# Kernel optimization log

Hardware: AMD Instinct MI355X
Metric: run time of the kernel (lower is better)

The kernel has to match this reference:

```python
import jax, jax.numpy as jnp
import numpy as np

N_NODES = 100000
N_EDGES = 3200000
D_IN, D_HID, D_OUT = 64, 16, 32


def setup_inputs() -> dict:
    key = jax.random.key(0)
    k1, k2, k3, k4, k5 = jax.random.split(key, 5)
    x = jax.random.normal(k1, (N_NODES, D_IN), dtype=jnp.float32)
    edge_index = jax.random.randint(k2, (2, N_EDGES), 0, N_NODES, dtype=jnp.int64)
    edge_weight = jax.random.uniform(k3, (N_EDGES,), dtype=jnp.float32)
    # Learned params (GCNConv lin has no bias; conv bias added post-aggregation)
    W_gcn = jax.random.normal(k4, (D_IN, D_HID), dtype=jnp.float32) / np.sqrt(D_IN)
    b_gcn = jnp.zeros((D_HID,), dtype=jnp.float32)
    W_out = jax.random.normal(k5, (D_HID, D_OUT), dtype=jnp.float32) / np.sqrt(D_HID)
    b_out = jnp.zeros((D_OUT,), dtype=jnp.float32)
    return {"x": x, "edge_index": edge_index, "edge_weight": edge_weight,
            "W_gcn": W_gcn, "b_gcn": b_gcn, "W_out": W_out, "b_out": b_out}


def reference(x, edge_index, edge_weight, W_gcn, b_gcn, W_out, b_out):
    N = x.shape[0]
    # --- gcn_norm with self loops (PyG defaults: add_self_loops=True, fill=1) ---
    loop = jnp.arange(N, dtype=edge_index.dtype)
    row = jnp.concatenate([edge_index[0], loop])  # source
    col = jnp.concatenate([edge_index[1], loop])  # target
    w = jnp.concatenate([edge_weight, jnp.ones((N,), dtype=x.dtype)])
    deg = jax.ops.segment_sum(w, col, num_segments=N)  # in-degree at targets
    dinv = jnp.where(deg > 0, jax.lax.rsqrt(deg), 0.0).astype(x.dtype)
    norm = dinv[row] * w * dinv[col]  # [E+N]
    # --- transform then gather / scatter-add aggregation ---
    h = x @ W_gcn                      # [N, 16]
    msg = h[row] * norm[:, None]       # [E+N, 16]
    agg = jax.ops.segment_sum(msg, col, num_segments=N) + b_gcn
    emb = jax.nn.relu(agg)
    return emb @ W_out + b_out         # [N, 32]
```

## Files before the change

### kernel.cpp

```cpp
#include <hip/hip_runtime.h>

#define D_IN  64
#define D_HID 16
#define D_OUT 32

#define CPB    64
#define CPB_SH 6
#define NB_MAX 1600
#define BINB   128

__global__ __launch_bounds__(256) void k_bincount(
        const int* __restrict__ col, int* __restrict__ cntB, int E, int NB) {
    __shared__ int hist[NB_MAX];
    for (int b = threadIdx.x; b < NB; b += 256) hist[b] = 0;
    __syncthreads();
    int chunk = (E + BINB - 1) / BINB;
    int s = blockIdx.x * chunk;
    int e = min(E, s + chunk);
    for (int i = s + threadIdx.x; i < e; i += 256)
        atomicAdd(&hist[col[i] >> CPB_SH], 1);
    __syncthreads();
    for (int b = threadIdx.x; b < NB; b += 256)
        cntB[b * BINB + blockIdx.x] = hist[b];
}

__global__ __launch_bounds__(BINB) void k_scanblk(int* __restrict__ cntB,
                                                  int* __restrict__ bb, int NB) {
    __shared__ int s[BINB];
    int b = blockIdx.x;
    int v = cntB[(size_t)b * BINB + threadIdx.x];
    s[threadIdx.x] = v;
    __syncthreads();
    for (int off = 1; off < BINB; off <<= 1) {
        int t = (threadIdx.x >= off) ? s[threadIdx.x - off] : 0;
        __syncthreads();
        s[threadIdx.x] += t;
        __syncthreads();
    }
    cntB[(size_t)b * BINB + threadIdx.x] = s[threadIdx.x] - v;
    if (threadIdx.x == BINB - 1) bb[b] = s[BINB - 1];
}

__global__ void k_scanbase(int* __restrict__ bb, int NB) {
    __shared__ int s[512];
    __shared__ int basev;
    if (threadIdx.x == 0) basev = 0;
    __syncthreads();
    for (int start = 0; start < NB; start += 512) {
        int idx = start + threadIdx.x;
        int v = (idx < NB) ? bb[idx] : 0;
        s[threadIdx.x] = v;
        __syncthreads();
        for (int off = 1; off < 512; off <<= 1) {
            int t = (threadIdx.x >= off) ? s[threadIdx.x - off] : 0;
            __syncthreads();
            s[threadIdx.x] += t;
            __syncthreads();
        }
        if (idx < NB) bb[idx] = basev + s[threadIdx.x] - v;
        __syncthreads();
        if (threadIdx.x == 0) basev += s[511];
        __syncthreads();
    }
    if (threadIdx.x == 0) bb[NB] = basev;
}

__global__ __launch_bounds__(256) void k_binfill(
        const int* __restrict__ ei, const float* __restrict__ w,
        const int* __restrict__ bb, const int* __restrict__ cntB,
        int2* __restrict__ binned, int E, int NB) {
    __shared__ int cur[NB_MAX];
    for (int b = threadIdx.x; b < NB; b += 256)
        cur[b] = bb[b] + cntB[(size_t)b * BINB + blockIdx.x];
    __syncthreads();
    int chunk = (E + BINB - 1) / BINB;
    int s = blockIdx.x * chunk;
    int e = min(E, s + chunk);
    for (int i = s + threadIdx.x; i < e; i += 256) {
        int c = ei[(size_t)E + i];
        int r = ei[i];
        float wt = w[i];
        int pos = atomicAdd(&cur[c >> CPB_SH], 1);
        binned[pos] = make_int2(r | ((c & (CPB - 1)) << 20), __float_as_int(wt));
    }
}

__global__ __launch_bounds__(256) void k_deg(
        const int2* __restrict__ binned, const int* __restrict__ bb,
        float* __restrict__ dinv, int N) {
    __shared__ float wsum[CPB];
    if (threadIdx.x < CPB) wsum[threadIdx.x] = 0.f;
    __syncthreads();
    int b = blockIdx.x;
    int s = bb[b], e = bb[b + 1];
    for (int i = s + threadIdx.x; i < e; i += 256) {
        int2 v = binned[i];
        atomicAdd(&wsum[(v.x >> 20) & (CPB - 1)], __int_as_float(v.y));
    }
    __syncthreads();
    if (threadIdx.x < CPB) {
        int n = (b << CPB_SH) + threadIdx.x;
        if (n < N) dinv[n] = rsqrtf(1.0f + wsum[threadIdx.x]);
    }
}

__global__ __launch_bounds__(256) void k_transform(
        const float4* __restrict__ x4,
        const float* __restrict__ Wg,
        const float* __restrict__ dinv,
        float* __restrict__ hs, int N) {
    __shared__ float Wl[D_IN * D_HID];
    __shared__ float xlf[16][68];
    for (int i = threadIdx.x; i < D_IN * D_HID; i += 256) Wl[i] = Wg[i];
    const int f = threadIdx.x & 15, nl = threadIdx.x >> 4;
    for (int base = blockIdx.x * 16; base < N; base += gridDim.x * 16) {
        __syncthreads();
        int n = base + nl;
        if (n < N) {
            float4 v = x4[(size_t)n * 16 + f];
            xlf[nl][f * 4 + 0] = v.x;
            xlf[nl][f * 4 + 1] = v.y;
            xlf[nl][f * 4 + 2] = v.z;
            xlf[nl][f * 4 + 3] = v.w;
        }
        __syncthreads();
        if (n < N) {
            float acc = 0.f;
#pragma unroll
            for (int k = 0; k < D_IN; ++k) acc += xlf[nl][k] * Wl[k * D_HID + f];
            hs[(size_t)n * D_HID + f] = acc * dinv[n];
        }
    }
}

__global__ __launch_bounds__(256) void k_aggout(
        const int2* __restrict__ binned, const int* __restrict__ bb,
        const float* __restrict__ hs, const float* __restrict__ dinv,
        const float* __restrict__ bg, const float* __restrict__ Wo,
        const float* __restrict__ bo, float* __restrict__ out, int N) {
    __shared__ float acc[CPB][D_HID + 1];
    __shared__ float Wl[D_HID * D_OUT];
    __shared__ float bgl[D_HID];
    __shared__ float bol[D_OUT];
    for (int i = threadIdx.x; i < CPB * (D_HID + 1); i += 256)
        ((float*)acc)[i] = 0.f;
    for (int i = threadIdx.x; i < D_HID * D_OUT; i += 256) Wl[i] = Wo[i];
    if (threadIdx.x < D_HID) bgl[threadIdx.x] = bg[threadIdx.x];
    if (threadIdx.x < D_OUT) bol[threadIdx.x] = bo[threadIdx.x];
    __syncthreads();

    int b = blockIdx.x;
    int s = bb[b], e = bb[b + 1];
    const int f = threadIdx.x & 15;
    int i = s + (threadIdx.x >> 4);
    for (; i + 16 < e; i += 32) {
        int2 v0 = binned[i];
        int2 v1 = binned[i + 16];
        float h0 = hs[(size_t)(v0.x & 0xFFFFF) * D_HID + f];
        float h1 = hs[(size_t)(v1.x & 0xFFFFF) * D_HID + f];
        atomicAdd(&acc[(v0.x >> 20) & (CPB - 1)][f], h0 * __int_as_float(v0.y));
        atomicAdd(&acc[(v1.x >> 20) & (CPB - 1)][f], h1 * __int_as_float(v1.y));
    }
    if (i < e) {
        int2 v = binned[i];
        float h = hs[(size_t)(v.x & 0xFFFFF) * D_HID + f];
        atomicAdd(&acc[(v.x >> 20) & (CPB - 1)][f], h * __int_as_float(v.y));
    }
    __syncthreads();

    {
        const int nl = threadIdx.x >> 4;
#pragma unroll
        for (int rep = 0; rep < CPB / 16; ++rep) {
            int cl = nl + rep * 16;
            int n = (b << CPB_SH) + cl;
            if (n < N) {
                float di = dinv[n];
                float v = di * (acc[cl][f] + hs[(size_t)n * D_HID + f]) + bgl[f];
                acc[cl][f] = fmaxf(v, 0.f);
            }
        }
    }
    __syncthreads();

    {
        const int o  = threadIdx.x & 31;
        const int n2 = threadIdx.x >> 5;
#pragma unroll
        for (int rep = 0; rep < CPB / 8; ++rep) {
            int cl = n2 + rep * 8;
            int n = (b << CPB_SH) + cl;
            if (n < N) {
                float a = bol[o];
#pragma unroll
                for (int ff = 0; ff < D_HID; ++ff)
                    a += acc[cl][ff] * Wl[ff * D_OUT + o];
                out[(size_t)n * D_OUT + o] = a;
            }
        }
    }
}

extern "C" void kernel_launch(void* const* d_in, const int* in_sizes, int n_in,
                              void* d_out, int out_size, void* d_ws, size_t ws_size,
                              hipStream_t stream) {
    const float* x  = (const float*)d_in[0];
    const int*   ei = (const int*)d_in[1];
    const float* ew = (const float*)d_in[2];
    const float* Wg = (const float*)d_in[3];
    const float* bg = (const float*)d_in[4];
    const float* Wo = (const float*)d_in[5];
    const float* bo = (const float*)d_in[6];
    float* out = (float*)d_out;

    const int N  = in_sizes[0] / D_IN;
    const int E  = in_sizes[2];
    const int NB = (N + CPB - 1) >> CPB_SH;

    float* ws    = (float*)d_ws;
    float* dinv  = ws;
    int*   bb    = (int*)(ws + N);
    size_t bbe   = (size_t)N + (size_t)((NB + 2) & ~1);
    int2*  binned = (int2*)(ws + bbe);
    float* hs    = ws + bbe + (size_t)2 * E;
    int*   cntB  = (int*)hs;

    k_bincount<<<BINB, 256, 0, stream>>>(ei + E, cntB, E, NB);
    k_scanblk <<<NB, BINB, 0, stream>>>(cntB, bb, NB);
    k_scanbase<<<1, 512, 0, stream>>>(bb, NB);
    k_binfill <<<BINB, 256, 0, stream>>>(ei, ew, bb, cntB, binned, E, NB);
    k_deg     <<<NB, 256, 0, stream>>>(binned, bb, dinv, N);
    k_transform<<<(N + 15) / 16, 256, 0, stream>>>((const float4*)x, Wg, dinv, hs, N);
    k_aggout  <<<NB, 256, 0, stream>>>(binned, bb, hs, dinv, bg, Wo, bo, out, N);
}
```

Before: 558.8 us.

## Bin edges by source band then target block, with nontemporal loads

Edges are now binned first by a band of the source node index (32768 nodes per band) and then by target block. Each aggregation block walks its bins band by band, so the gathered rows of hs from all blocks fall in a narrower address range at any given time, which is meant to improve cache locality. Streaming reads of edge_index, weights and binned entries now use nontemporal loads, and the binning grid is cut from 128 to 64 blocks. The trade-offs are a larger histogram (up to 6400 bins in LDS), more scan work, and fewer blocks in the bincount and binfill kernels.

New measurement: 728.8 us. +30.4%, slower.

```diff
diff --git a/kernel.cpp b/kernel.cpp
--- a/kernel.cpp
+++ b/kernel.cpp
@@ -4,28 +4,40 @@
 #define D_HID 16
 #define D_OUT 32
 
-#define CPB    64
-#define CPB_SH 6
-#define NB_MAX 1600
-#define BINB   128
+#define CPB      64
+#define CPB_SH   6
+#define BAND_SH  15
+#define NBIN_MAX 6400
+#define BINB     64
+
+static __device__ __forceinline__ long long ntld_ll(const void* p) {
+    return __builtin_nontemporal_load((const long long*)p);
+}
+static __device__ __forceinline__ int ntld_i(const int* p) {
+    return __builtin_nontemporal_load(p);
+}
 
 __global__ __launch_bounds__(256) void k_bincount(
-        const int* __restrict__ col, int* __restrict__ cntB, int E, int NB) {
-    __shared__ int hist[NB_MAX];
-    for (int b = threadIdx.x; b < NB; b += 256) hist[b] = 0;
+        const int* __restrict__ ei, int* __restrict__ cntB,
+        int E, int NB, int NBIN) {
+    __shared__ int hist[NBIN_MAX];
+    for (int b = threadIdx.x; b < NBIN; b += 256) hist[b] = 0;
     __syncthreads();
     int chunk = (E + BINB - 1) / BINB;
     int s = blockIdx.x * chunk;
     int e = min(E, s + chunk);
-    for (int i = s + threadIdx.x; i < e; i += 256)
-        atomicAdd(&hist[col[i] >> CPB_SH], 1);
-    __syncthreads();
-    for (int b = threadIdx.x; b < NB; b += 256)
-        cntB[b * BINB + blockIdx.x] = hist[b];
+    for (int i = s + threadIdx.x; i < e; i += 256) {
+        int r = ntld_i(ei + i);
+        int c = ntld_i(ei + E + i);
+        atomicAdd(&hist[(r >> BAND_SH) * NB + (c >> CPB_SH)], 1);
+    }
+    __syncthreads();
+    for (int b = threadIdx.x; b < NBIN; b += 256)
+        cntB[(size_t)b * BINB + blockIdx.x] = hist[b];
 }
 
 __global__ __launch_bounds__(BINB) void k_scanblk(int* __restrict__ cntB,
-                                                  int* __restrict__ bb, int NB) {
+                                                  int* __restrict__ bb, int NBIN) {
     __shared__ int s[BINB];
     int b = blockIdx.x;
     int v = cntB[(size_t)b * BINB + threadIdx.x];
@@ -41,14 +53,14 @@
     if (threadIdx.x == BINB - 1) bb[b] = s[BINB - 1];
 }
 
-__global__ void k_scanbase(int* __restrict__ bb, int NB) {
+__global__ void k_scanbase(int* __restrict__ bb, int NBIN) {
     __shared__ int s[512];
     __shared__ int basev;
     if (threadIdx.x == 0) basev = 0;
     __syncthreads();
-    for (int start = 0; start < NB; start += 512) {
+    for (int start = 0; start < NBIN; start += 512) {
         int idx = start + threadIdx.x;
-        int v = (idx < NB) ? bb[idx] : 0;
+        int v = (idx < NBIN) ? bb[idx] : 0;
         s[threadIdx.x] = v;
         __syncthreads();
         for (int off = 1; off < 512; off <<= 1) {
@@ -57,45 +69,49 @@
             s[threadIdx.x] += t;
             __syncthreads();
         }
-        if (idx < NB) bb[idx] = basev + s[threadIdx.x] - v;
+        if (idx < NBIN) bb[idx] = basev + s[threadIdx.x] - v;
         __syncthreads();
         if (threadIdx.x == 0) basev += s[511];
         __syncthreads();
     }
-    if (threadIdx.x == 0) bb[NB] = basev;
+    if (threadIdx.x == 0) bb[NBIN] = basev;
 }
 
 __global__ __launch_bounds__(256) void k_binfill(
         const int* __restrict__ ei, const float* __restrict__ w,
         const int* __restrict__ bb, const int* __restrict__ cntB,
-        int2* __restrict__ binned, int E, int NB) {
-    __shared__ int cur[NB_MAX];
-    for (int b = threadIdx.x; b < NB; b += 256)
+        int2* __restrict__ binned, int E, int NB, int NBIN) {
+    __shared__ int cur[NBIN_MAX];
+    for (int b = threadIdx.x; b < NBIN; b += 256)
         cur[b] = bb[b] + cntB[(size_t)b * BINB + blockIdx.x];
     __syncthreads();
     int chunk = (E + BINB - 1) / BINB;
     int s = blockIdx.x * chunk;
     int e = min(E, s + chunk);
     for (int i = s + threadIdx.x; i < e; i += 256) {
-        int c = ei[(size_t)E + i];
-        int r = ei[i];
-        float wt = w[i];
-        int pos = atomicAdd(&cur[c >> CPB_SH], 1);
+        int r = ntld_i(ei + i);
+        int c = ntld_i(ei + E + i);
+        float wt = __builtin_nontemporal_load(w + i);
+        int bin = (r >> BAND_SH) * NB + (c >> CPB_SH);
+        int pos = atomicAdd(&cur[bin], 1);
         binned[pos] = make_int2(r | ((c & (CPB - 1)) << 20), __float_as_int(wt));
     }
 }
 
 __global__ __launch_bounds__(256) void k_deg(
         const int2* __restrict__ binned, const int* __restrict__ bb,
-        float* __restrict__ dinv, int N) {
+        float* __restrict__ dinv, int N, int NB, int nband) {
     __shared__ float wsum[CPB];
     if (threadIdx.x < CPB) wsum[threadIdx.x] = 0.f;
     __syncthreads();
     int b = blockIdx.x;
-    int s = bb[b], e = bb[b + 1];
-    for (int i = s + threadIdx.x; i < e; i += 256) {
-        int2 v = binned[i];
-        atomicAdd(&wsum[(v.x >> 20) & (CPB - 1)], __int_as_float(v.y));
+    for (int band = 0; band < nband; ++band) {
+        int bs = bb[band * NB + b], be = bb[band * NB + b + 1];
+        for (int i = bs + threadIdx.x; i < be; i += 256) {
+            long long p = ntld_ll(binned + i);
+            atomicAdd(&wsum[((int)p >> 20) & (CPB - 1)],
+                      __int_as_float((int)(p >> 32)));
+        }
     }
     __syncthreads();
     if (threadIdx.x < CPB) {
@@ -137,7 +153,8 @@
         const int2* __restrict__ binned, const int* __restrict__ bb,
         const float* __restrict__ hs, const float* __restrict__ dinv,
         const float* __restrict__ bg, const float* __restrict__ Wo,
-        const float* __restrict__ bo, float* __restrict__ out, int N) {
+        const float* __restrict__ bo, float* __restrict__ out,
+        int N, int NB, int nband) {
     __shared__ float acc[CPB][D_HID + 1];
     __shared__ float Wl[D_HID * D_OUT];
     __shared__ float bgl[D_HID];
@@ -150,21 +167,29 @@
     __syncthreads();
 
     int b = blockIdx.x;
-    int s = bb[b], e = bb[b + 1];
     const int f = threadIdx.x & 15;
-    int i = s + (threadIdx.x >> 4);
-    for (; i + 16 < e; i += 32) {
-        int2 v0 = binned[i];
-        int2 v1 = binned[i + 16];
-        float h0 = hs[(size_t)(v0.x & 0xFFFFF) * D_HID + f];
-        float h1 = hs[(size_t)(v1.x & 0xFFFFF) * D_HID + f];
-        atomicAdd(&acc[(v0.x >> 20) & (CPB - 1)][f], h0 * __int_as_float(v0.y));
-        atomicAdd(&acc[(v1.x >> 20) & (CPB - 1)][f], h1 * __int_as_float(v1.y));
-    }
-    if (i < e) {
-        int2 v = binned[i];
-        float h = hs[(size_t)(v.x & 0xFFFFF) * D_HID + f];
-        atomicAdd(&acc[(v.x >> 20) & (CPB - 1)][f], h * __int_as_float(v.y));
+    const int slot = threadIdx.x >> 4;
+    for (int band = 0; band < nband; ++band) {
+        int bs = bb[band * NB + b], be = bb[band * NB + b + 1];
+        int i = bs + slot;
+        for (; i + 16 < be; i += 32) {
+            long long p0 = ntld_ll(binned + i);
+            long long p1 = ntld_ll(binned + i + 16);
+            int r0 = (int)p0, r1 = (int)p1;
+            float h0 = hs[(size_t)(r0 & 0xFFFFF) * D_HID + f];
+            float h1 = hs[(size_t)(r1 & 0xFFFFF) * D_HID + f];
+            atomicAdd(&acc[(r0 >> 20) & (CPB - 1)][f],
+                      h0 * __int_as_float((int)(p0 >> 32)));
+            atomicAdd(&acc[(r1 >> 20) & (CPB - 1)][f],
+                      h1 * __int_as_float((int)(p1 >> 32)));
+        }
+        if (i < be) {
+            long long p = ntld_ll(binned + i);
+            int r = (int)p;
+            float h = hs[(size_t)(r & 0xFFFFF) * D_HID + f];
+            atomicAdd(&acc[(r >> 20) & (CPB - 1)][f],
+                      h * __int_as_float((int)(p >> 32)));
+        }
     }
     __syncthreads();
 
@@ -213,23 +238,26 @@
     const float* bo = (const float*)d_in[6];
     float* out = (float*)d_out;
 
-    const int N  = in_sizes[0] / D_IN;
-    const int E  = in_sizes[2];
-    const int NB = (N + CPB - 1) >> CPB_SH;
-
-    float* ws    = (float*)d_ws;
-    float* dinv  = ws;
-    int*   bb    = (int*)(ws + N);
-    size_t bbe   = (size_t)N + (size_t)((NB + 2) & ~1);
+    const int N     = in_sizes[0] / D_IN;
+    const int E     = in_sizes[2];
+    const int NB    = (N + CPB - 1) >> CPB_SH;
+    const int nband = (N + (1 << BAND_SH) - 1) >> BAND_SH;
+    const int NBIN  = nband * NB;
+
+    float* ws     = (float*)d_ws;
+    float* dinv   = ws;
+    int*   bb     = (int*)(ws + N);
+    size_t bbe    = (size_t)N + (size_t)((NBIN + 2) & ~1);
     int2*  binned = (int2*)(ws + bbe);
-    float* hs    = ws + bbe + (size_t)2 * E;
-    int*   cntB  = (int*)hs;
-
-    k_bincount<<<BINB, 256, 0, stream>>>(ei + E, cntB, E, NB);
-    k_scanblk <<<NB, BINB, 0, stream>>>(cntB, bb, NB);
-    k_scanbase<<<1, 512, 0, stream>>>(bb, NB);
-    k_binfill <<<BINB, 256, 0, stream>>>(ei, ew, bb, cntB, binned, E, NB);
-    k_deg     <<<NB, 256, 0, stream>>>(binned, bb, dinv, N);
+    float* hs     = ws + bbe + (size_t)2 * E;
+    int*   cntB   = (int*)hs;
+
+    k_bincount<<<BINB, 256, 0, stream>>>(ei, cntB, E, NB, NBIN);
+    k_scanblk <<<NBIN, BINB, 0, stream>>>(cntB, bb, NBIN);
+    k_scanbase<<<1, 512, 0, stream>>>(bb, NBIN);
+    k_binfill <<<BINB, 256, 0, stream>>>(ei, ew, bb, cntB, binned, E, NB, NBIN);
+    k_deg     <<<NB, 256, 0, stream>>>(binned, bb, dinv, N, NB, nband);
     k_transform<<<(N + 15) / 16, 256, 0, stream>>>((const float4*)x, Wg, dinv, hs, N);
-    k_aggout  <<<NB, 256, 0, stream>>>(binned, bb, hs, dinv, bg, Wo, bo, out, N);
-}
+    k_aggout  <<<NB, 256, 0, stream>>>(binned, bb, hs, dinv, bg, Wo, bo, out,
+                                       N, NB, nband);
+}
```

## Sub-sort each column bin by source band to localize hs gathers

Applied to the files above, without the earlier changes.

The degree kernel becomes a per-bin band sort. It stages each bin's edges in LDS, counts them by source-row band (4096 rows), and scatters them back grouped by band, recording band offsets. The aggregation kernel walks the bands in order, so concurrently running blocks tend to gather hs rows from similar regions, which should improve L2 locality. The change also adds nontemporal loads for streamed edge data, at the cost of an extra read and write pass over the binned edges plus large LDS usage that may reduce occupancy of the sort kernel.

Result: slower. 594.0 us (+6.3%).

```diff
diff --git a/kernel.cpp b/kernel.cpp
--- a/kernel.cpp
+++ b/kernel.cpp
@@ -4,10 +4,20 @@
 #define D_HID 16
 #define D_OUT 32
 
-#define CPB    64
-#define CPB_SH 6
-#define NB_MAX 1600
-#define BINB   128
+#define CPB      64
+#define CPB_SH   6
+#define NB_MAX   1600
+#define BINB     128
+#define BAND2_SH 12
+#define KB_MAX   32
+#define SEG_CAP  6144
+
+static __device__ __forceinline__ long long ntld_ll(const void* p) {
+    return __builtin_nontemporal_load((const long long*)p);
+}
+static __device__ __forceinline__ int ntld_i(const int* p) {
+    return __builtin_nontemporal_load(p);
+}
 
 __global__ __launch_bounds__(256) void k_bincount(
         const int* __restrict__ col, int* __restrict__ cntB, int E, int NB) {
@@ -18,10 +28,10 @@
     int s = blockIdx.x * chunk;
     int e = min(E, s + chunk);
     for (int i = s + threadIdx.x; i < e; i += 256)
-        atomicAdd(&hist[col[i] >> CPB_SH], 1);
+        atomicAdd(&hist[ntld_i(col + i) >> CPB_SH], 1);
     __syncthreads();
     for (int b = threadIdx.x; b < NB; b += 256)
-        cntB[b * BINB + blockIdx.x] = hist[b];
+        cntB[(size_t)b * BINB + blockIdx.x] = hist[b];
 }
 
 __global__ __launch_bounds__(BINB) void k_scanblk(int* __restrict__ cntB,
@@ -77,25 +87,56 @@
     int s = blockIdx.x * chunk;
     int e = min(E, s + chunk);
     for (int i = s + threadIdx.x; i < e; i += 256) {
-        int c = ei[(size_t)E + i];
-        int r = ei[i];
-        float wt = w[i];
+        int r = ntld_i(ei + i);
+        int c = ntld_i(ei + E + i);
+        float wt = __builtin_nontemporal_load(w + i);
         int pos = atomicAdd(&cur[c >> CPB_SH], 1);
         binned[pos] = make_int2(r | ((c & (CPB - 1)) << 20), __float_as_int(wt));
     }
 }
 
-__global__ __launch_bounds__(256) void k_deg(
-        const int2* __restrict__ binned, const int* __restrict__ bb,
-        float* __restrict__ dinv, int N) {
+__global__ __launch_bounds__(256) void k_bandsort(
+        int2* __restrict__ binned, const int* __restrict__ bb,
+        int* __restrict__ bb2, float* __restrict__ dinv, int N, int kb) {
+    __shared__ int2  seg[SEG_CAP];
     __shared__ float wsum[CPB];
+    __shared__ int   cnt2[KB_MAX + 1];
+    __shared__ int   cur2[KB_MAX];
+    int b = blockIdx.x;
+    int s = bb[b], e = bb[b + 1], len = e - s;
     if (threadIdx.x < CPB) wsum[threadIdx.x] = 0.f;
-    __syncthreads();
-    int b = blockIdx.x;
-    int s = bb[b], e = bb[b + 1];
-    for (int i = s + threadIdx.x; i < e; i += 256) {
-        int2 v = binned[i];
-        atomicAdd(&wsum[(v.x >> 20) & (CPB - 1)], __int_as_float(v.y));
+    if (threadIdx.x <= kb) cnt2[threadIdx.x] = 0;
+    __syncthreads();
+
+    if (len <= SEG_CAP) {
+        for (int j = threadIdx.x; j < len; j += 256) {
+            int2 v = binned[s + j];
+            seg[j] = v;
+            atomicAdd(&wsum[(v.x >> 20) & (CPB - 1)], __int_as_float(v.y));
+            atomicAdd(&cnt2[(v.x & 0xFFFFF) >> BAND2_SH], 1);
+        }
+        __syncthreads();
+        if (threadIdx.x == 0) {
+            int run = s;
+            for (int k = 0; k < kb; ++k) { int c = cnt2[k]; cnt2[k] = run; run += c; }
+            cnt2[kb] = run;
+        }
+        __syncthreads();
+        if (threadIdx.x < kb)  cur2[threadIdx.x] = cnt2[threadIdx.x];
+        if (threadIdx.x <= kb) bb2[(size_t)b * (kb + 1) + threadIdx.x] = cnt2[threadIdx.x];
+        __syncthreads();
+        for (int j = threadIdx.x; j < len; j += 256) {
+            int2 v = seg[j];
+            int pos = atomicAdd(&cur2[(v.x & 0xFFFFF) >> BAND2_SH], 1);
+            binned[pos] = v;
+        }
+    } else {
+        for (int j = threadIdx.x; j < len; j += 256) {
+            int2 v = binned[s + j];
+            atomicAdd(&wsum[(v.x >> 20) & (CPB - 1)], __int_as_float(v.y));
+        }
+        if (threadIdx.x <= kb)
+            bb2[(size_t)b * (kb + 1) + threadIdx.x] = (threadIdx.x == 0) ? s : e;
     }
     __syncthreads();
     if (threadIdx.x < CPB) {
@@ -105,10 +146,8 @@
 }
 
 __global__ __launch_bounds__(256) void k_transform(
-        const float4* __restrict__ x4,
-        const float* __restrict__ Wg,
-        const float* __restrict__ dinv,
-        float* __restrict__ hs, int N) {
+        const float4* __restrict__ x4, const float* __restrict__ Wg,
+        const float* __restrict__ dinv, float* __restrict__ hs, int N) {
     __shared__ float Wl[D_IN * D_HID];
     __shared__ float xlf[16][68];
     for (int i = threadIdx.x; i < D_IN * D_HID; i += 256) Wl[i] = Wg[i];
@@ -134,10 +173,10 @@
 }
 
 __global__ __launch_bounds__(256) void k_aggout(
-        const int2* __restrict__ binned, const int* __restrict__ bb,
+        const int2* __restrict__ binned, const int* __restrict__ bb2,
         const float* __restrict__ hs, const float* __restrict__ dinv,
         const float* __restrict__ bg, const float* __restrict__ Wo,
-        const float* __restrict__ bo, float* __restrict__ out, int N) {
+        const float* __restrict__ bo, float* __restrict__ out, int N, int kb) {
     __shared__ float acc[CPB][D_HID + 1];
     __shared__ float Wl[D_HID * D_OUT];
     __shared__ float bgl[D_HID];
@@ -150,21 +189,30 @@
     __syncthreads();
 
     int b = blockIdx.x;
-    int s = bb[b], e = bb[b + 1];
     const int f = threadIdx.x & 15;
-    int i = s + (threadIdx.x >> 4);
-    for (; i + 16 < e; i += 32) {
-        int2 v0 = binned[i];
-        int2 v1 = binned[i + 16];
-        float h0 = hs[(size_t)(v0.x & 0xFFFFF) * D_HID + f];
-        float h1 = hs[(size_t)(v1.x & 0xFFFFF) * D_HID + f];
-        atomicAdd(&acc[(v0.x >> 20) & (CPB - 1)][f], h0 * __int_as_float(v0.y));
-        atomicAdd(&acc[(v1.x >> 20) & (CPB - 1)][f], h1 * __int_as_float(v1.y));
-    }
-    if (i < e) {
-        int2 v = binned[i];
-        float h = hs[(size_t)(v.x & 0xFFFFF) * D_HID + f];
-        atomicAdd(&acc[(v.x >> 20) & (CPB - 1)][f], h * __int_as_float(v.y));
+    const int slot = threadIdx.x >> 4;
+    for (int k = 0; k < kb; ++k) {
+        int bs = bb2[(size_t)b * (kb + 1) + k];
+        int be = bb2[(size_t)b * (kb + 1) + k + 1];
+        int i = bs + slot;
+        for (; i + 16 < be; i += 32) {
+            long long p0 = ntld_ll(binned + i);
+            long long p1 = ntld_ll(binned + i + 16);
+            int r0 = (int)p0, r1 = (int)p1;
+            float h0 = hs[(size_t)(r0 & 0xFFFFF) * D_HID + f];
+            float h1 = hs[(size_t)(r1 & 0xFFFFF) * D_HID + f];
+            atomicAdd(&acc[(r0 >> 20) & (CPB - 1)][f],
+                      h0 * __int_as_float((int)(p0 >> 32)));
+            atomicAdd(&acc[(r1 >> 20) & (CPB - 1)][f],
+                      h1 * __int_as_float((int)(p1 >> 32)));
+        }
+        if (i < be) {
+            long long p = ntld_ll(binned + i);
+            int r = (int)p;
+            float h = hs[(size_t)(r & 0xFFFFF) * D_HID + f];
+            atomicAdd(&acc[(r >> 20) & (CPB - 1)][f],
+                      h * __int_as_float((int)(p >> 32)));
+        }
     }
     __syncthreads();
 
@@ -216,20 +264,23 @@
     const int N  = in_sizes[0] / D_IN;
     const int E  = in_sizes[2];
     const int NB = (N + CPB - 1) >> CPB_SH;
-
-    float* ws    = (float*)d_ws;
-    float* dinv  = ws;
-    int*   bb    = (int*)(ws + N);
-    size_t bbe   = (size_t)N + (size_t)((NB + 2) & ~1);
-    int2*  binned = (int2*)(ws + bbe);
-    float* hs    = ws + bbe + (size_t)2 * E;
-    int*   cntB  = (int*)hs;
+    const int kb = (N + (1 << BAND2_SH) - 1) >> BAND2_SH;
+
+    float* ws   = (float*)d_ws;
+    float* dinv = ws;
+    int*   bb   = (int*)(ws + N);
+    size_t o2   = (size_t)N + (size_t)((NB + 2) & ~1);
+    int*   bb2  = (int*)(ws + o2);
+    size_t o3   = o2 + (((size_t)NB * (kb + 1) + 1) & ~(size_t)1);
+    int2*  binned = (int2*)(ws + o3);
+    float* hs   = ws + o3 + (size_t)2 * E;
+    int*   cntB = (int*)hs;
 
     k_bincount<<<BINB, 256, 0, stream>>>(ei + E, cntB, E, NB);
     k_scanblk <<<NB, BINB, 0, stream>>>(cntB, bb, NB);
     k_scanbase<<<1, 512, 0, stream>>>(bb, NB);
     k_binfill <<<BINB, 256, 0, stream>>>(ei, ew, bb, cntB, binned, E, NB);
-    k_deg     <<<NB, 256, 0, stream>>>(binned, bb, dinv, N);
+    k_bandsort<<<NB, 256, 0, stream>>>(binned, bb, bb2, dinv, N, kb);
     k_transform<<<(N + 15) / 16, 256, 0, stream>>>((const float4*)x, Wg, dinv, hs, N);
-    k_aggout  <<<NB, 256, 0, stream>>>(binned, bb, hs, dinv, bg, Wo, bo, out, N);
-}
+    k_aggout  <<<NB, 256, 0, stream>>>(binned, bb2, hs, dinv, bg, Wo, bo, out, N, kb);
+}
```
